# Optimization experiments

Hardware: AMD Instinct MI355X
Metric: run time of the kernel (lower is better)

Reference implementation:

```python
import jax, jax.numpy as jnp
import numpy as np

B, S, D = 2, 2048, 2048
NH, NKV, HD = 16, 4, 128
EPS = 1e-6


def rmsnorm(x, w, eps=EPS):
    # torch.nn.RMSNorm: x * rsqrt(mean(x^2) + eps) * weight
    ms = jnp.mean(jnp.square(x), axis=-1, keepdims=True)
    return x * jax.lax.rsqrt(ms + eps) * w


def apply_rotary_emb(x, freqs_cis):
    # x: (B, S, H, HD); freqs_cis: (S, HD//2, 2) -> pairwise complex rotation (gpt-fast style)
    xs = x.reshape(*x.shape[:-1], -1, 2)          # (B,S,H,HD//2,2)
    fc = freqs_cis[None, :, None, :, :]           # (1,S,1,HD//2,2)
    xr, xi = xs[..., 0], xs[..., 1]
    fr, fi = fc[..., 0], fc[..., 1]
    out = jnp.stack([xr * fr - xi * fi, xi * fr + xr * fi], axis=-1)
    return out.reshape(x.shape)


def setup_inputs() -> dict:
    key = jax.random.key(0)
    ks = jax.random.split(key, 4)
    x = jax.random.normal(ks[0], (B, S, D), dtype=jnp.float32)
    freqs_cis = jax.random.normal(ks[1], (S, HD // 2, 2), dtype=jnp.float32)
    wqkv = jax.random.normal(ks[2], ((NH + 2 * NKV) * HD, D), dtype=jnp.float32) * (D ** -0.5)
    wo = jax.random.normal(ks[3], (NH * HD, D), dtype=jnp.float32).T * ((NH * HD) ** -0.5)
    wo = jnp.asarray(wo)  # (D, NH*HD) torch layout (out,in)
    q_norm_w = jnp.ones((HD,), dtype=jnp.float32)
    k_norm_w = jnp.ones((HD,), dtype=jnp.float32)
    return {"x": x, "freqs_cis": freqs_cis, "wqkv": wqkv, "wo": wo,
            "q_norm_w": q_norm_w, "k_norm_w": k_norm_w}


def reference(x, freqs_cis, wqkv, wo, q_norm_w, k_norm_w):
    b, s, _ = x.shape
    q_size, kv_size = NH * HD, NKV * HD
    qkv = jnp.einsum('bsd,ed->bse', x, wqkv)  # fused QKV projection
    q, k, v = jnp.split(qkv, [q_size, q_size + kv_size], axis=-1)
    q = q.reshape(b, s, NH, HD)
    k = k.reshape(b, s, NKV, HD)
    v = v.reshape(b, s, NKV, HD)
    q = rmsnorm(q, q_norm_w)
    k = rmsnorm(k, k_norm_w)
    q = apply_rotary_emb(q, freqs_cis)
    k = apply_rotary_emb(k, freqs_cis)
    # GQA: repeat_interleave KV heads to NH
    rep = NH // NKV
    k = jnp.repeat(k, rep, axis=2)  # (b,s,NH,HD)
    v = jnp.repeat(v, rep, axis=2)
    scale = 1.0 / np.sqrt(HD)
    scores = jnp.einsum('bqhd,bkhd->bhqk', q, k) * scale
    causal = jnp.tril(jnp.ones((s, s), dtype=bool))
    scores = jnp.where(causal[None, None], scores, -jnp.inf)
    attn = jax.nn.softmax(scores, axis=-1)
    y = jnp.einsum('bhqk,bkhd->bqhd', attn, v)
    y = y.reshape(b, s, q_size)
    return jnp.einsum('bse,de->bsd', y, wo)
```

## Files before the change

### kernel.cpp

```cpp
#include <hip/hip_runtime.h>
#include <math.h>

constexpr int B_ = 2, S_ = 2048, D_ = 2048, NH_ = 16, NKV_ = 4, HD_ = 128;
constexpr int EQKV_ = (NH_ + 2 * NKV_) * HD_;
constexpr int M_ = B_ * S_;
constexpr float EPS_ = 1e-6f;
constexpr float QSCALE_ = 0.08838834764831845f;

typedef __attribute__((ext_vector_type(8))) short bf16x8;
typedef __attribute__((ext_vector_type(4))) float f32x4;
typedef __attribute__((address_space(1))) unsigned int gu32;
typedef __attribute__((address_space(3))) unsigned int lu32;

__device__ inline ushort f2bf(float f) {
    unsigned u = __float_as_uint(f);
    return (ushort)((u + 0x7FFF + ((u >> 16) & 1)) >> 16);
}

__global__ __launch_bounds__(256) void pack_bf16(
    const float* __restrict__ in, ushort* __restrict__ out, int n4)
{
    int i = blockIdx.x * 256 + threadIdx.x;
    if (i >= n4) return;
    float4 f = ((const float4*)in)[i];
    ushort4 u;
    u.x = f2bf(f.x); u.y = f2bf(f.y); u.z = f2bf(f.z); u.w = f2bf(f.w);
    ((ushort4*)out)[i] = u;
}

__global__ __launch_bounds__(256) void gemm_nt_bf16(
    const ushort* __restrict__ A, const ushort* __restrict__ W,
    float* __restrict__ C, int M, int N, int K)
{
    __shared__ ushort As[128 * 32];
    __shared__ ushort Bs[128 * 32];
    const int t = threadIdx.x;
    const int wave = t >> 6, lane = t & 63;
    const int m0 = blockIdx.y * 128, n0 = blockIdx.x * 128;
    const int wm = (wave >> 1) * 64, wn = (wave & 1) * 64;
    const int lrow = lane & 15, lquad = lane >> 4;

    f32x4 acc[4][4];
#pragma unroll
    for (int i = 0; i < 4; ++i)
#pragma unroll
        for (int j = 0; j < 4; ++j) acc[i][j] = (f32x4){0.f, 0.f, 0.f, 0.f};

    for (int k0 = 0; k0 < K; k0 += 32) {
        __syncthreads();
#pragma unroll
        for (int i = 0; i < 2; ++i) {
            int chunk = t + 256 * i;
            int row = chunk >> 2, seg = chunk & 3;
            int ubase = (wave * 64 + 256 * i) * 8;
            __builtin_amdgcn_global_load_lds(
                (const gu32*)(A + (size_t)(m0 + row) * K + k0 + seg * 8),
                (lu32*)(As + ubase), 16, 0, 0);
            __builtin_amdgcn_global_load_lds(
                (const gu32*)(W + (size_t)(n0 + row) * K + k0 + seg * 8),
                (lu32*)(Bs + ubase), 16, 0, 0);
        }
        __syncthreads();

        bf16x8 af[4], bf[4];
#pragma unroll
        for (int i = 0; i < 4; ++i) {
            af[i] = *(const bf16x8*)(As + (wm + i * 16 + lrow) * 32 + lquad * 8);
            bf[i] = *(const bf16x8*)(Bs + (wn + i * 16 + lrow) * 32 + lquad * 8);
        }
#pragma unroll
        for (int i = 0; i < 4; ++i)
#pragma unroll
            for (int j = 0; j < 4; ++j)
                acc[i][j] = __builtin_amdgcn_mfma_f32_16x16x32_bf16(
                    af[i], bf[j], acc[i][j], 0, 0, 0);
    }
#pragma unroll
    for (int i = 0; i < 4; ++i)
#pragma unroll
        for (int j = 0; j < 4; ++j) {
            float* cp = C + (size_t)(m0 + wm + i * 16 + lquad * 4) * N
                          + n0 + wn + j * 16 + lrow;
#pragma unroll
            for (int r = 0; r < 4; ++r) cp[(size_t)r * N] = acc[i][j][r];
        }
}

__global__ __launch_bounds__(256) void gemm_qkv_fused(
    const ushort* __restrict__ A,
    const ushort* __restrict__ W,
    const float* __restrict__ freqs,
    const float* __restrict__ qw, const float* __restrict__ kw,
    ushort* __restrict__ qo, ushort* __restrict__ ko, ushort* __restrict__ vo,
    int K)
{
    __shared__ __align__(16) ushort smem[128 * 136];
    __shared__ float rsbuf[256];
    ushort* As = smem;
    ushort* Bs = smem + 4096;
    ushort* Lt = smem;

    const int t = threadIdx.x;
    const int wave = t >> 6, lane = t & 63;
    const int m0 = blockIdx.y * 128, n0 = blockIdx.x * 128;
    const int wm = (wave >> 1) * 64, wn = (wave & 1) * 64;
    const int half = wave & 1;
    const int lrow = lane & 15, lquad = lane >> 4;
    const int head = n0 >> 7;
    const int b = m0 >> 11, s0 = m0 & (S_ - 1);

    f32x4 acc[4][4];
#pragma unroll
    for (int i = 0; i < 4; ++i)
#pragma unroll
        for (int j = 0; j < 4; ++j) acc[i][j] = (f32x4){0.f, 0.f, 0.f, 0.f};

    for (int k0 = 0; k0 < K; k0 += 32) {
        __syncthreads();
#pragma unroll
        for (int i = 0; i < 2; ++i) {
            int chunk = t + 256 * i;
            int row = chunk >> 2, seg = chunk & 3;
            int ubase = (wave * 64 + 256 * i) * 8;
            __builtin_amdgcn_global_load_lds(
                (const gu32*)(A + (size_t)(m0 + row) * K + k0 + seg * 8),
                (lu32*)(As + ubase), 16, 0, 0);
            __builtin_amdgcn_global_load_lds(
                (const gu32*)(W + (size_t)(n0 + row) * K + k0 + seg * 8),
                (lu32*)(Bs + ubase), 16, 0, 0);
        }
        __syncthreads();

        bf16x8 af[4], bf[4];
#pragma unroll
        for (int i = 0; i < 4; ++i) {
            af[i] = *(const bf16x8*)(As + (wm + i * 16 + lrow) * 32 + lquad * 8);
            bf[i] = *(const bf16x8*)(Bs + (wn + i * 16 + lrow) * 32 + lquad * 8);
        }
#pragma unroll
        for (int i = 0; i < 4; ++i)
#pragma unroll
            for (int j = 0; j < 4; ++j)
                acc[i][j] = __builtin_amdgcn_mfma_f32_16x16x32_bf16(
                    af[i], bf[j], acc[i][j], 0, 0, 0);
    }
    __syncthreads();

    float part[4][4];
    if (head < NH_ + NKV_) {
#pragma unroll
        for (int i = 0; i < 4; ++i)
#pragma unroll
            for (int r = 0; r < 4; ++r) {
                float p = acc[i][0][r] * acc[i][0][r]
                        + acc[i][1][r] * acc[i][1][r]
                        + acc[i][2][r] * acc[i][2][r]
                        + acc[i][3][r] * acc[i][3][r];
#pragma unroll
                for (int off = 1; off < 16; off <<= 1) p += __shfl_xor(p, off);
                part[i][r] = p;
                if (lrow == 0)
                    rsbuf[half * 128 + wm + i * 16 + lquad * 4 + r] = p;
            }
    }
    __syncthreads();

    if (head < NH_ + NKV_) {
        const float* nw = (head < NH_) ? qw : kw;
        float wv[4];
#pragma unroll
        for (int j = 0; j < 4; ++j) wv[j] = nw[wn + j * 16 + lrow];
#pragma unroll
        for (int i = 0; i < 4; ++i)
#pragma unroll
            for (int r = 0; r < 4; ++r) {
                const int rowid = wm + i * 16 + lquad * 4 + r;
                const int s = s0 + rowid;
                const float total = part[i][r] + rsbuf[(half ^ 1) * 128 + rowid];
                const float rs = rsqrtf(total * (1.0f / HD_) + EPS_);
#pragma unroll
                for (int j = 0; j < 4; ++j) {
                    const int d = wn + j * 16 + lrow;
                    const float xn = acc[i][j][r] * rs * wv[j];
                    const float other = __shfl_xor(xn, 1);
                    const float fr = freqs[s * HD_ + (d & ~1)];
                    const float fi = freqs[s * HD_ + (d & ~1) + 1];
                    float out = (d & 1) ? fmaf(xn, fr, other * fi)
                                        : fmaf(xn, fr, -other * fi);
                    if (head < NH_) out *= QSCALE_;
                    Lt[rowid * 136 + d] = f2bf(out);
                }
            }
    } else {
#pragma unroll
        for (int i = 0; i < 4; ++i)
#pragma unroll
            for (int j = 0; j < 4; ++j)
#pragma unroll
                for (int r = 0; r < 4; ++r)
                    Lt[(wn + j * 16 + lrow) * 136 + wm + i * 16 + lquad * 4 + r]
                        = f2bf(acc[i][j][r]);
    }
    __syncthreads();

    const int g = t >> 4, lx16 = t & 15;
    if (head < NH_) {
        ushort* dst0 = qo + ((size_t)(b * NH_ + head) * S_ + s0) * HD_;
#pragma unroll
        for (int it = 0; it < 8; ++it) {
            const int rowid = it * 16 + g;
            uint4 v = *(const uint4*)(Lt + rowid * 136 + lx16 * 8);
            *(uint4*)(dst0 + (size_t)rowid * HD_ + lx16 * 8) = v;
        }
    } else if (head < NH_ + NKV_) {
        const int kh = head - NH_;
        ushort* dst0 = ko + ((size_t)(b * NKV_ + kh) * S_ + s0) * HD_;
#pragma unroll
        for (int it = 0; it < 8; ++it) {
            const int rowid = it * 16 + g;
            uint4 v = *(const uint4*)(Lt + rowid * 136 + lx16 * 8);
            *(uint4*)(dst0 + (size_t)rowid * HD_ + lx16 * 8) = v;
        }
    } else {
        const int vh = head - (NH_ + NKV_);
        ushort* dst0 = vo + ((size_t)(b * NKV_ + vh) * HD_) * S_ + s0;
#pragma unroll
        for (int it = 0; it < 8; ++it) {
            const int rowid = it * 16 + g;
            uint4 v = *(const uint4*)(Lt + rowid * 136 + lx16 * 8);
            *(uint4*)(dst0 + (size_t)rowid * S_ + lx16 * 8) = v;
        }
    }
}

__global__ __launch_bounds__(256, 3) void flash_attn_mfma(
    const ushort* __restrict__ Q,
    const ushort* __restrict__ K,
    const ushort* __restrict__ V,
    ushort* __restrict__ Y,
    float* __restrict__ OP,
    float* __restrict__ ML)
{
    __shared__ __align__(16) ushort Ks[4 * 64 * 32];
    __shared__ __align__(16) ushort Vs[2 * 128 * 32];
    __shared__ __align__(16) ushort Ps[4 * 16 * 72];

    const int t = threadIdx.x, w = t >> 6, lane = t & 63;
    const int lx = lane & 15, quad = lane >> 4;
    const int h = blockIdx.y, b = blockIdx.z;

    const int gx = blockIdx.x;
    int qt, halfsel, tk0, tk1;
    bool split;
    if (gx < 32) {
        split = true;
        qt = 31 - (gx >> 1);
        halfsel = gx & 1;
        const int nt = qt + 1, nt0 = nt >> 1;
        tk0 = halfsel ? nt0 : 0;
        tk1 = halfsel ? nt : nt0;
    } else {
        split = false;
        qt = 47 - gx;
        halfsel = 0;
        tk0 = 0;
        tk1 = qt + 1;
    }
    const int q0 = qt * 64;
    const int kvh = h >> 2;
    const int srow = lane >> 2, sseg = lane & 3;
    const int wslot = (sseg ^ ((srow >> 1) & 3)) * 8;
    const int rslot = (quad ^ ((lx >> 1) & 3)) * 8;

    const ushort* qb = Q + ((size_t)(b * NH_ + h) * S_ + q0) * HD_;
    const ushort* ksrc = K + ((size_t)(b * NKV_ + kvh) * S_ + w * 16 + srow) * HD_
                           + sseg * 8;
    const ushort* vb = V + ((size_t)(b * NKV_ + kvh) * HD_) * S_;
    const ushort* vsrc0 = vb + (size_t)(w * 16 + srow) * S_ + sseg * 8;
    const ushort* vsrc1 = vb + (size_t)(64 + w * 16 + srow) * S_ + sseg * 8;
    ushort* kdst = Ks + w * 512 + srow * 32 + wslot;
    ushort* vdst0 = Vs + (w * 16 + srow) * 32 + wslot;
    ushort* vdst1 = Vs + (64 + w * 16 + srow) * 32 + wslot;

    bf16x8 aq[4];
#pragma unroll
    for (int ks = 0; ks < 4; ++ks)
        aq[ks] = *(const bf16x8*)(qb + (size_t)(w * 16 + lx) * HD_ + ks * 32 + quad * 8);

    f32x4 o[8];
#pragma unroll
    for (int j = 0; j < 8; ++j) o[j] = (f32x4){0.f, 0.f, 0.f, 0.f};
    float mrow[4] = {-INFINITY, -INFINITY, -INFINITY, -INFINITY};
    float lp[4] = {0.f, 0.f, 0.f, 0.f};

    uint4 kr0, kr1, kr2, kr3, vr0, vr1, vr2, vr3;
    {
        const size_t kb0 = (size_t)tk0 * 64;
        kr0 = *(const uint4*)(ksrc + kb0 * HD_ +  0);
        kr1 = *(const uint4*)(ksrc + kb0 * HD_ + 32);
        kr2 = *(const uint4*)(ksrc + kb0 * HD_ + 64);
        kr3 = *(const uint4*)(ksrc + kb0 * HD_ + 96);
        vr0 = *(const uint4*)(vsrc0 + kb0 +  0);
        vr1 = *(const uint4*)(vsrc1 + kb0 +  0);
        vr2 = *(const uint4*)(vsrc0 + kb0 + 32);
        vr3 = *(const uint4*)(vsrc1 + kb0 + 32);
    }

    for (int tk = tk0; tk < tk1; ++tk) {
        const int k0 = tk * 64;
        asm volatile("s_barrier" ::: "memory");
        *(uint4*)(kdst +    0) = kr0;
        *(uint4*)(kdst + 2048) = kr1;
        *(uint4*)(kdst + 4096) = kr2;
        *(uint4*)(kdst + 6144) = kr3;
        *(uint4*)(vdst0 +    0) = vr0;
        *(uint4*)(vdst1 +    0) = vr1;
        *(uint4*)(vdst0 + 4096) = vr2;
        *(uint4*)(vdst1 + 4096) = vr3;
        asm volatile("s_waitcnt lgkmcnt(0)" ::: "memory");
        asm volatile("s_barrier" ::: "memory");

        if (tk + 1 < tk1) {
            const size_t ko8 = (size_t)(k0 + 64);
            kr0 = *(const uint4*)(ksrc + ko8 * HD_ +  0);
            kr1 = *(const uint4*)(ksrc + ko8 * HD_ + 32);
            kr2 = *(const uint4*)(ksrc + ko8 * HD_ + 64);
            kr3 = *(const uint4*)(ksrc + ko8 * HD_ + 96);
            vr0 = *(const uint4*)(vsrc0 + ko8 +  0);
            vr1 = *(const uint4*)(vsrc1 + ko8 +  0);
            vr2 = *(const uint4*)(vsrc0 + ko8 + 32);
            vr3 = *(const uint4*)(vsrc1 + ko8 + 32);
        }

        f32x4 s[4];
#pragma unroll
        for (int j = 0; j < 4; ++j) s[j] = (f32x4){0.f, 0.f, 0.f, 0.f};
        __builtin_amdgcn_s_setprio(1);
#pragma unroll
        for (int ks = 0; ks < 4; ++ks) {
#pragma unroll
            for (int j = 0; j < 4; ++j) {
                bf16x8 bk = *(const bf16x8*)(Ks + ks * 2048 + (j * 16 + lx) * 32 + rslot);
                s[j] = __builtin_amdgcn_mfma_f32_16x16x32_bf16(aq[ks], bk, s[j], 0, 0, 0);
            }
        }
        __builtin_amdgcn_s_setprio(0);

        const int qrow_base = q0 + w * 16 + quad * 4;
        if (tk == qt) {
#pragma unroll
            for (int reg = 0; reg < 4; ++reg) {
                const int qrow = qrow_base + reg;
#pragma unroll
                for (int j = 0; j < 4; ++j)
                    if (k0 + lx + 16 * j > qrow) s[j][reg] = -INFINITY;
            }
        }

        float rmx[4];
        bool need = false;
#pragma unroll
        for (int reg = 0; reg < 4; ++reg) {
            rmx[reg] = fmaxf(fmaxf(s[0][reg], s[1][reg]),
                             fmaxf(s[2][reg], s[3][reg]));
            need |= (rmx[reg] > mrow[reg] + 8.0f);
        }
        if (__any(need)) {
#pragma unroll
            for (int reg = 0; reg < 4; ++reg) {
                float rm = rmx[reg];
#pragma unroll
                for (int off = 1; off < 16; off <<= 1)
                    rm = fmaxf(rm, __shfl_xor(rm, off));
                const float mn = fmaxf(mrow[reg], rm);
                const float alpha = __expf(mrow[reg] - mn);
                mrow[reg] = mn;
                lp[reg] *= alpha;
#pragma unroll
                for (int j = 0; j < 8; ++j) o[j][reg] *= alpha;
            }
        }
#pragma unroll
        for (int reg = 0; reg < 4; ++reg) {
#pragma unroll
            for (int j = 0; j < 4; ++j) {
                const float p = __expf(s[j][reg] - mrow[reg]);
                lp[reg] += p;
                Ps[w * 1152 + (quad * 4 + reg) * 72 + lx + 16 * j] = f2bf(p);
            }
        }

        bf16x8 ap[2];
#pragma unroll
        for (int ks2 = 0; ks2 < 2; ++ks2)
            ap[ks2] = *(const bf16x8*)(Ps + w * 1152 + lx * 72 + ks2 * 32 + quad * 8);
        __builtin_amdgcn_s_setprio(1);
#pragma unroll
        for (int jd = 0; jd < 8; ++jd) {
#pragma unroll
            for (int ks2 = 0; ks2 < 2; ++ks2) {
                bf16x8 bv = *(const bf16x8*)(Vs + ks2 * 4096 + (jd * 16 + lx) * 32 + rslot);
                o[jd] = __builtin_amdgcn_mfma_f32_16x16x32_bf16(ap[ks2], bv, o[jd], 0, 0, 0);
            }
        }
        __builtin_amdgcn_s_setprio(0);
    }

#pragma unroll
    for (int reg = 0; reg < 4; ++reg) {
        float l = lp[reg];
#pragma unroll
        for (int off = 1; off < 16; off <<= 1) l += __shfl_xor(l, off);
        lp[reg] = l;
    }
    if (!split) {
#pragma unroll
        for (int reg = 0; reg < 4; ++reg) {
            const float inv = 1.0f / lp[reg];
            const size_t yb = (size_t)(b * S_ + q0 + w * 16 + quad * 4 + reg) * (NH_ * HD_)
                            + h * HD_ + lx;
#pragma unroll
            for (int jd = 0; jd < 8; ++jd)
                Y[yb + jd * 16] = f2bf(o[jd][reg] * inv);
        }
    } else {
        const int bh = b * NH_ + h;
        const int st = qt - 16;
        const size_t pidx = (size_t)(bh * 16 + st) * 2 + halfsel;
        float* mlb = ML + pidx * 128;
#pragma unroll
        for (int reg = 0; reg < 4; ++reg) {
            const int row = w * 16 + quad * 4 + reg;
            if (lx == 0) {
                mlb[row] = mrow[reg];
                mlb[64 + row] = lp[reg];
            }
            float* ob = OP + (pidx * 64 + row) * 128 + lx;
#pragma unroll
            for (int jd = 0; jd < 8; ++jd)
                ob[jd * 16] = o[jd][reg];
        }
    }
}

__global__ __launch_bounds__(256) void attn_combine(
    const float* __restrict__ OP, const float* __restrict__ ML,
    ushort* __restrict__ Y)
{
    const int st = blockIdx.x, h = blockIdx.y, b = blockIdx.z;
    const int bh = b * NH_ + h;
    const int d = threadIdx.x & 127, rg = threadIdx.x >> 7;
    const size_t p0 = (size_t)(bh * 16 + st) * 2;
    const float* ml0 = ML + p0 * 128;
    const float* ml1 = ML + (p0 + 1) * 128;
    const float* o0 = OP + p0 * 64 * 128;
    const float* o1 = OP + (p0 + 1) * 64 * 128;
    const int q0 = (16 + st) * 64;
#pragma unroll
    for (int r = rg; r < 64; r += 2) {
        const float m0 = ml0[r], l0 = ml0[64 + r];
        const float m1 = ml1[r], l1 = ml1[64 + r];
        const float m = fmaxf(m0, m1);
        const float w0 = __expf(m0 - m), w1 = __expf(m1 - m);
        const float inv = 1.0f / (l0 * w0 + l1 * w1);
        const float v = (o0[r * 128 + d] * w0 + o1[r * 128 + d] * w1) * inv;
        Y[((size_t)(b * S_ + q0 + r)) * (NH_ * HD_) + h * HD_ + d] = f2bf(v);
    }
}

extern "C" void kernel_launch(void* const* d_in, const int* in_sizes, int n_in,
                              void* d_out, int out_size, void* d_ws, size_t ws_size,
                              hipStream_t stream)
{
    const float* x     = (const float*)d_in[0];
    const float* freqs = (const float*)d_in[1];
    const float* wqkv  = (const float*)d_in[2];
    const float* wo    = (const float*)d_in[3];
    const float* qw    = (const float*)d_in[4];
    const float* kw    = (const float*)d_in[5];
    float* out = (float*)d_out;

    char* ws = (char*)d_ws;
    ushort* qbf    = (ushort*)(ws + 0);
    ushort* kbf    = (ushort*)(ws + 16777216);
    ushort* vtb    = (ushort*)(ws + 20971520);
    ushort* ybf    = (ushort*)(ws + 25165824);
    ushort* wobf   = (ushort*)(ws + 41943040);
    ushort* wqkvbf = (ushort*)(ws + 50331648);
    ushort* xbf    = (ushort*)(ws + 83886080);
    float*  OP     = (float*)(ws + 50331648);
    float*  ML     = (float*)(ws + 83886080);

    pack_bf16<<<(M_ * D_ / 4 + 255) / 256, 256, 0, stream>>>(x, xbf, M_ * D_ / 4);
    pack_bf16<<<(EQKV_ * D_ / 4 + 255) / 256, 256, 0, stream>>>(wqkv, wqkvbf,
                                                                EQKV_ * D_ / 4);
    gemm_qkv_fused<<<dim3(EQKV_ / 128, M_ / 128), 256, 0, stream>>>(
        xbf, wqkvbf, freqs, qw, kw, qbf, kbf, vtb, D_);
    pack_bf16<<<(D_ * NH_ * HD_ / 4 + 255) / 256, 256, 0, stream>>>(
        wo, wobf, D_ * NH_ * HD_ / 4);
    flash_attn_mfma<<<dim3(48, NH_, B_), 256, 0, stream>>>(qbf, kbf, vtb, ybf,
                                                           OP, ML);
    attn_combine<<<dim3(16, NH_, B_), 256, 0, stream>>>(OP, ML, ybf);
    gemm_nt_bf16<<<dim3(D_ / 128, M_ / 128), 256, 0, stream>>>(
        ybf, wobf, out, M_, D_, NH_ * HD_);
}
```

Before: 349.5 us.

## Enlarge flash-attention query tile to 128 rows with 8 waves per block

```diff
diff --git a/kernel.cpp b/kernel.cpp
--- a/kernel.cpp
+++ b/kernel.cpp
@@ -233,7 +233,7 @@
     }
 }
 
-__global__ __launch_bounds__(256, 3) void flash_attn_mfma(
+__global__ __launch_bounds__(512, 6) void flash_attn_mfma(
     const ushort* __restrict__ Q,
     const ushort* __restrict__ K,
     const ushort* __restrict__ V,
@@ -243,49 +243,50 @@
 {
     __shared__ __align__(16) ushort Ks[4 * 64 * 32];
     __shared__ __align__(16) ushort Vs[2 * 128 * 32];
-    __shared__ __align__(16) ushort Ps[4 * 16 * 72];
+    __shared__ __align__(16) ushort Ps[8 * 16 * 72];
 
     const int t = threadIdx.x, w = t >> 6, lane = t & 63;
     const int lx = lane & 15, quad = lane >> 4;
     const int h = blockIdx.y, b = blockIdx.z;
 
     const int gx = blockIdx.x;
-    int qt, halfsel, tk0, tk1;
+    int qb, halfsel, tk0, tk1;
     bool split;
-    if (gx < 32) {
+    if (gx < 22) {
         split = true;
-        qt = 31 - (gx >> 1);
+        qb = 15 - (gx >> 1);
         halfsel = gx & 1;
-        const int nt = qt + 1, nt0 = nt >> 1;
-        tk0 = halfsel ? nt0 : 0;
-        tk1 = halfsel ? nt : nt0;
+        const int h0 = qb + 1;
+        tk0 = halfsel ? h0 : 0;
+        tk1 = halfsel ? 2 * qb + 2 : h0;
     } else {
         split = false;
-        qt = 47 - gx;
+        qb = 26 - gx;
         halfsel = 0;
         tk0 = 0;
-        tk1 = qt + 1;
-    }
-    const int q0 = qt * 64;
+        tk1 = 2 * qb + 2;
+    }
+    const int q0 = qb * 128;
     const int kvh = h >> 2;
-    const int srow = lane >> 2, sseg = lane & 3;
-    const int wslot = (sseg ^ ((srow >> 1) & 3)) * 8;
+
+    const int srow8 = lane >> 3, sseg8 = lane & 7;
+    const int fsw = (srow8 >> 1) & 3;
+    const int slotw = ((sseg8 & 3) ^ fsw) * 8;
+    const int krow = w * 8 + srow8;
+    const int d0 = w * 8 + srow8;
+    ushort* kdst = Ks + (sseg8 >> 2) * 2048 + krow * 32 + slotw;
+    ushort* vdst = Vs + (sseg8 >> 2) * 4096 + d0 * 32 + slotw;
+    const ushort* ksrc = K + ((size_t)(b * NKV_ + kvh) * S_ + krow) * HD_
+                           + sseg8 * 8;
+    const ushort* vsrc = V + ((size_t)(b * NKV_ + kvh) * HD_ + d0) * S_
+                           + sseg8 * 8;
     const int rslot = (quad ^ ((lx >> 1) & 3)) * 8;
 
-    const ushort* qb = Q + ((size_t)(b * NH_ + h) * S_ + q0) * HD_;
-    const ushort* ksrc = K + ((size_t)(b * NKV_ + kvh) * S_ + w * 16 + srow) * HD_
-                           + sseg * 8;
-    const ushort* vb = V + ((size_t)(b * NKV_ + kvh) * HD_) * S_;
-    const ushort* vsrc0 = vb + (size_t)(w * 16 + srow) * S_ + sseg * 8;
-    const ushort* vsrc1 = vb + (size_t)(64 + w * 16 + srow) * S_ + sseg * 8;
-    ushort* kdst = Ks + w * 512 + srow * 32 + wslot;
-    ushort* vdst0 = Vs + (w * 16 + srow) * 32 + wslot;
-    ushort* vdst1 = Vs + (64 + w * 16 + srow) * 32 + wslot;
-
+    const ushort* qb_ = Q + ((size_t)(b * NH_ + h) * S_ + q0) * HD_;
     bf16x8 aq[4];
 #pragma unroll
     for (int ks = 0; ks < 4; ++ks)
-        aq[ks] = *(const bf16x8*)(qb + (size_t)(w * 16 + lx) * HD_ + ks * 32 + quad * 8);
+        aq[ks] = *(const bf16x8*)(qb_ + (size_t)(w * 16 + lx) * HD_ + ks * 32 + quad * 8);
 
     f32x4 o[8];
 #pragma unroll
@@ -293,43 +294,31 @@
     float mrow[4] = {-INFINITY, -INFINITY, -INFINITY, -INFINITY};
     float lp[4] = {0.f, 0.f, 0.f, 0.f};
 
-    uint4 kr0, kr1, kr2, kr3, vr0, vr1, vr2, vr3;
+    uint4 kr0, kr1, vr0, vr1;
     {
-        const size_t kb0 = (size_t)tk0 * 64;
-        kr0 = *(const uint4*)(ksrc + kb0 * HD_ +  0);
-        kr1 = *(const uint4*)(ksrc + kb0 * HD_ + 32);
-        kr2 = *(const uint4*)(ksrc + kb0 * HD_ + 64);
-        kr3 = *(const uint4*)(ksrc + kb0 * HD_ + 96);
-        vr0 = *(const uint4*)(vsrc0 + kb0 +  0);
-        vr1 = *(const uint4*)(vsrc1 + kb0 +  0);
-        vr2 = *(const uint4*)(vsrc0 + kb0 + 32);
-        vr3 = *(const uint4*)(vsrc1 + kb0 + 32);
+        const size_t kf = (size_t)tk0 * 64;
+        kr0 = *(const uint4*)(ksrc + kf * HD_);
+        kr1 = *(const uint4*)(ksrc + kf * HD_ + 64);
+        vr0 = *(const uint4*)(vsrc + kf);
+        vr1 = *(const uint4*)(vsrc + (size_t)64 * S_ + kf);
     }
 
     for (int tk = tk0; tk < tk1; ++tk) {
         const int k0 = tk * 64;
         asm volatile("s_barrier" ::: "memory");
         *(uint4*)(kdst +    0) = kr0;
-        *(uint4*)(kdst + 2048) = kr1;
-        *(uint4*)(kdst + 4096) = kr2;
-        *(uint4*)(kdst + 6144) = kr3;
-        *(uint4*)(vdst0 +    0) = vr0;
-        *(uint4*)(vdst1 +    0) = vr1;
-        *(uint4*)(vdst0 + 4096) = vr2;
-        *(uint4*)(vdst1 + 4096) = vr3;
+        *(uint4*)(kdst + 4096) = kr1;
+        *(uint4*)(vdst +    0) = vr0;
+        *(uint4*)(vdst + 2048) = vr1;
         asm volatile("s_waitcnt lgkmcnt(0)" ::: "memory");
         asm volatile("s_barrier" ::: "memory");
 
         if (tk + 1 < tk1) {
-            const size_t ko8 = (size_t)(k0 + 64);
-            kr0 = *(const uint4*)(ksrc + ko8 * HD_ +  0);
-            kr1 = *(const uint4*)(ksrc + ko8 * HD_ + 32);
-            kr2 = *(const uint4*)(ksrc + ko8 * HD_ + 64);
-            kr3 = *(const uint4*)(ksrc + ko8 * HD_ + 96);
-            vr0 = *(const uint4*)(vsrc0 + ko8 +  0);
-            vr1 = *(const uint4*)(vsrc1 + ko8 +  0);
-            vr2 = *(const uint4*)(vsrc0 + ko8 + 32);
-            vr3 = *(const uint4*)(vsrc1 + ko8 + 32);
+            const size_t kf = (size_t)(k0 + 64);
+            kr0 = *(const uint4*)(ksrc + kf * HD_);
+            kr1 = *(const uint4*)(ksrc + kf * HD_ + 64);
+            vr0 = *(const uint4*)(vsrc + kf);
+            vr1 = *(const uint4*)(vsrc + (size_t)64 * S_ + kf);
         }
 
         f32x4 s[4];
@@ -347,7 +336,7 @@
         __builtin_amdgcn_s_setprio(0);
 
         const int qrow_base = q0 + w * 16 + quad * 4;
-        if (tk == qt) {
+        if (k0 + 63 > q0 + w * 16) {
 #pragma unroll
             for (int reg = 0; reg < 4; ++reg) {
                 const int qrow = qrow_base + reg;
@@ -424,18 +413,16 @@
                 Y[yb + jd * 16] = f2bf(o[jd][reg] * inv);
         }
     } else {
-        const int bh = b * NH_ + h;
-        const int st = qt - 16;
-        const size_t pidx = (size_t)(bh * 16 + st) * 2 + halfsel;
-        float* mlb = ML + pidx * 128;
+        const int sp = ((b * NH_ + h) * 11 + (qb - 5)) * 2 + halfsel;
+        float* mlb = ML + (size_t)sp * 256;
 #pragma unroll
         for (int reg = 0; reg < 4; ++reg) {
             const int row = w * 16 + quad * 4 + reg;
             if (lx == 0) {
                 mlb[row] = mrow[reg];
-                mlb[64 + row] = lp[reg];
-            }
-            float* ob = OP + (pidx * 64 + row) * 128 + lx;
+                mlb[128 + row] = lp[reg];
+            }
+            float* ob = OP + ((size_t)sp * 128 + row) * 128 + lx;
 #pragma unroll
             for (int jd = 0; jd < 8; ++jd)
                 ob[jd * 16] = o[jd][reg];
@@ -447,19 +434,19 @@
     const float* __restrict__ OP, const float* __restrict__ ML,
     ushort* __restrict__ Y)
 {
-    const int st = blockIdx.x, h = blockIdx.y, b = blockIdx.z;
-    const int bh = b * NH_ + h;
+    const int gx = blockIdx.x, h = blockIdx.y, b = blockIdx.z;
+    const int qb = 5 + gx;
+    const int q0 = qb * 128;
+    const int sp0 = ((b * NH_ + h) * 11 + gx) * 2;
+    const float* ml0 = ML + (size_t)sp0 * 256;
+    const float* ml1 = ML + (size_t)(sp0 + 1) * 256;
+    const float* o0 = OP + (size_t)sp0 * 128 * 128;
+    const float* o1 = OP + (size_t)(sp0 + 1) * 128 * 128;
     const int d = threadIdx.x & 127, rg = threadIdx.x >> 7;
-    const size_t p0 = (size_t)(bh * 16 + st) * 2;
-    const float* ml0 = ML + p0 * 128;
-    const float* ml1 = ML + (p0 + 1) * 128;
-    const float* o0 = OP + p0 * 64 * 128;
-    const float* o1 = OP + (p0 + 1) * 64 * 128;
-    const int q0 = (16 + st) * 64;
-#pragma unroll
-    for (int r = rg; r < 64; r += 2) {
-        const float m0 = ml0[r], l0 = ml0[64 + r];
-        const float m1 = ml1[r], l1 = ml1[64 + r];
+#pragma unroll
+    for (int r = rg; r < 128; r += 2) {
+        const float m0 = ml0[r], l0 = ml0[128 + r];
+        const float m1 = ml1[r], l1 = ml1[128 + r];
         const float m = fmaxf(m0, m1);
         const float w0 = __expf(m0 - m), w1 = __expf(m1 - m);
         const float inv = 1.0f / (l0 * w0 + l1 * w1);
@@ -489,7 +476,7 @@
     ushort* wqkvbf = (ushort*)(ws + 50331648);
     ushort* xbf    = (ushort*)(ws + 83886080);
     float*  OP     = (float*)(ws + 50331648);
-    float*  ML     = (float*)(ws + 83886080);
+    float*  ML     = (float*)(ws + 96468992);
 
     pack_bf16<<<(M_ * D_ / 4 + 255) / 256, 256, 0, stream>>>(x, xbf, M_ * D_ / 4);
     pack_bf16<<<(EQKV_ * D_ / 4 + 255) / 256, 256, 0, stream>>>(wqkv, wqkvbf,
@@ -498,9 +485,9 @@
         xbf, wqkvbf, freqs, qw, kw, qbf, kbf, vtb, D_);
     pack_bf16<<<(D_ * NH_ * HD_ / 4 + 255) / 256, 256, 0, stream>>>(
         wo, wobf, D_ * NH_ * HD_ / 4);
-    flash_attn_mfma<<<dim3(48, NH_, B_), 256, 0, stream>>>(qbf, kbf, vtb, ybf,
+    flash_attn_mfma<<<dim3(27, NH_, B_), 512, 0, stream>>>(qbf, kbf, vtb, ybf,
                                                            OP, ML);
-    attn_combine<<<dim3(16, NH_, B_), 256, 0, stream>>>(OP, ML, ybf);
+    attn_combine<<<dim3(11, NH_, B_), 256, 0, stream>>>(OP, ML, ybf);
     gemm_nt_bf16<<<dim3(D_ / 128, M_ / 128), 256, 0, stream>>>(
         ybf, wobf, out, M_, D_, NH_ * HD_);
 }
```

Measured after the change: 491.2 us. 1.41x slower.
